# Kernel tuning notes

Measured on AMD Instinct MI355X. Metric: run time of the kernel, lower is better.

Reference implementation:

```python
import jax, jax.numpy as jnp
import numpy as np
import math

B, C, H, L, E = 4, 4, 8, 512, 128  # L == win_size + 1


def setup_inputs() -> dict:
    key = jax.random.key(0)
    kq, kk, kv, ks = jax.random.split(key, 4)
    queries = jax.random.normal(kq, (B, C, H, L, E), jnp.float32)
    keys = jax.random.normal(kk, (B, C, H, L, E), jnp.float32)
    values = jax.random.normal(kv, (B, C, H, L, E), jnp.float32)
    sigma = jax.random.normal(ks, (B, C, H, L), jnp.float32)
    # triangular causal mask: True above the diagonal (masked out)
    tri = jnp.triu(jnp.ones((L, L), dtype=bool), k=1)
    attn_mask = jnp.broadcast_to(tri[None, None, None], (B, 1, 1, L, L))
    return {"queries": queries, "keys": keys, "values": values,
            "sigma": sigma, "attn_mask": attn_mask}


def reference(queries, keys, values, sigma, attn_mask):
    Bq, Cq, Hq, Lq, Eq = queries.shape
    scale = 1.0 / math.sqrt(Eq)
    # scores: [B,C,H,L,L]
    scores = jnp.einsum("bchle,bchme->bchlm", queries, keys)
    scores = jnp.where(attn_mask, -jnp.inf, scores)
    attn = scale * scores

    # Gaussian prior from learned sigma
    sig = jax.nn.sigmoid(sigma * 5.0) + 1e-5
    sig = jnp.power(3.0, sig) - 1.0            # [B,C,H,L]
    sig = sig[..., None]                        # [B,C,H,L,1]
    idx = jnp.arange(Lq, dtype=queries.dtype)
    dist = jnp.abs(idx[:, None] - idx[None, :])  # [L,L]
    inv_norm = 1.0 / (math.sqrt(2.0 * math.pi) * sig)
    prior = inv_norm * jnp.exp(-(dist ** 2) / (2.0 * sig ** 2))  # [B,C,H,L,L]

    series = jax.nn.softmax(attn, axis=-1)      # dropout p=0.0 -> identity
    V = jnp.einsum("bchlm,bchme->bchle", series, values)
    sigma_out = jnp.broadcast_to(sig, prior.shape)
    return V, series, prior, sigma_out
```

## Files before the change

kernel.cpp:

```cpp
#include <hip/hip_runtime.h>
#include <math.h>

#define L 512
#define E 128
#define NT 8

typedef __attribute__((ext_vector_type(8))) short bf16x8;
typedef __attribute__((ext_vector_type(4))) float f32x4;
typedef __attribute__((ext_vector_type(4))) unsigned short u16x4;

__device__ __forceinline__ unsigned short bf16_rne(float x) {
  unsigned u = __builtin_bit_cast(unsigned, x);
  unsigned r = u + 0x7FFFu + ((u >> 16) & 1u);
  return (unsigned short)(r >> 16);
}
__device__ __forceinline__ float bf16_to_f(unsigned short h) {
  unsigned u = ((unsigned)h) << 16;
  return __builtin_bit_cast(float, u);
}

__global__ __launch_bounds__(256) void prior_kernel(
    const float* __restrict__ sigma,
    float* __restrict__ prior,
    float* __restrict__ sigma_out) {
  const int half = threadIdx.x >> 7;
  const int t128 = threadIdx.x & 127;
  const int m0 = t128 * 4;
#pragma unroll 4
  for (int i = 0; i < 16; ++i) {
    const int row = blockIdx.x * 32 + i * 2 + half;
    const int l = row & (L - 1);
    const float x = sigma[row];
    const float sg = 1.0f / (1.0f + __expf(-5.0f * x)) + 1e-5f;
    const float sigp = expm1f(sg * 1.0986122886681098f);
    const float inv_norm = 0.3989422804014327f / sigp;
    const float c = -1.0f / (2.0f * sigp * sigp);

    f32x4 pr, so;
    so[0] = so[1] = so[2] = so[3] = sigp;
#pragma unroll
    for (int j = 0; j < 4; ++j) {
      float d = (float)(l - (m0 + j));
      pr[j] = inv_norm * __expf(c * d * d);
    }
    const size_t off = (size_t)row * L + m0;
    __builtin_nontemporal_store(pr, (f32x4*)(prior + off));
    __builtin_nontemporal_store(so, (f32x4*)(sigma_out + off));
  }
}

__global__ __launch_bounds__(256, 2) void attn_kernel(
    const float* __restrict__ Q,
    const float* __restrict__ K,
    const float* __restrict__ V,
    float* __restrict__ outV,
    float* __restrict__ series) {
  const int bch = blockIdx.x;
  const int qt = blockIdx.y;
  const int tid = threadIdx.x;
  const int w = tid >> 6, lane = tid & 63, r = lane & 15, g = lane >> 4;

  __shared__ char smem[34816];
  char* sKhi = smem;
  char* sKlo = smem + 17408;
  char* sP = smem;
  char* sVt = smem + 9216;

  const size_t base = (size_t)bch * (L * E);
  const int qbase = qt * 64;
  const float scale = 0.08838834764831845f;

  bf16x8 qh[4], ql[4];
  {
    const float* qrow = Q + base + (size_t)(qbase + 16 * w + r) * E;
#pragma unroll
    for (int ks = 0; ks < 4; ++ks) {
      const int e0 = 32 * ks + 8 * g;
      f32x4 a = *(const f32x4*)(qrow + e0);
      f32x4 b = *(const f32x4*)(qrow + e0 + 4);
#pragma unroll
      for (int j = 0; j < 4; ++j) {
        float xa = a[j] * scale;
        unsigned short ha = bf16_rne(xa);
        qh[ks][j] = (short)ha;
        ql[ks][j] = (short)bf16_rne(xa - bf16_to_f(ha));
        float xb = b[j] * scale;
        unsigned short hb = bf16_rne(xb);
        qh[ks][4 + j] = (short)hb;
        ql[ks][4 + j] = (short)bf16_rne(xb - bf16_to_f(hb));
      }
    }
  }

  f32x4 Sacc[NT][4];
#pragma unroll
  for (int t = 0; t < NT; ++t)
#pragma unroll
    for (int cb = 0; cb < 4; ++cb) Sacc[t][cb] = (f32x4){0.f, 0.f, 0.f, 0.f};

#pragma unroll
  for (int t = 0; t < NT; ++t) {
    if (t <= qt) {
      __syncthreads();
#pragma unroll
      for (int i = 0; i < 8; ++i) {
        int f = i * 256 + tid;
        int row = f >> 5;
        int e0 = (f & 31) * 4;
        f32x4 kv = *(const f32x4*)(K + base + (size_t)(t * 64 + row) * E + e0);
        u16x4 h4, l4;
#pragma unroll
        for (int j = 0; j < 4; ++j) {
          unsigned short h = bf16_rne(kv[j]);
          h4[j] = h;
          l4[j] = bf16_rne(kv[j] - bf16_to_f(h));
        }
        *(u16x4*)(sKhi + row * 272 + e0 * 2) = h4;
        *(u16x4*)(sKlo + row * 272 + e0 * 2) = l4;
      }
      __syncthreads();

#pragma unroll
      for (int ks = 0; ks < 4; ++ks) {
#pragma unroll
        for (int cb = 0; cb < 4; ++cb) {
          const int kb = (16 * cb + r) * 272 + (32 * ks + 8 * g) * 2;
          bf16x8 bh = *(const bf16x8*)(sKhi + kb);
          bf16x8 bl = *(const bf16x8*)(sKlo + kb);
          f32x4 acc = Sacc[t][cb];
          acc = __builtin_amdgcn_mfma_f32_16x16x32_bf16(qh[ks], bh, acc, 0, 0, 0);
          acc = __builtin_amdgcn_mfma_f32_16x16x32_bf16(ql[ks], bh, acc, 0, 0, 0);
          acc = __builtin_amdgcn_mfma_f32_16x16x32_bf16(qh[ks], bl, acc, 0, 0, 0);
          Sacc[t][cb] = acc;
        }
      }
    }
  }

  float mrow[4], srow[4], inv[4];
#pragma unroll
  for (int reg = 0; reg < 4; ++reg) mrow[reg] = -__builtin_inff();

#pragma unroll
  for (int t = 0; t < NT; ++t) {
    if (t > qt) continue;
#pragma unroll
    for (int cb = 0; cb < 4; ++cb)
#pragma unroll
      for (int reg = 0; reg < 4; ++reg) {
        float s = Sacc[t][cb][reg];
        if (t == qt && (16 * cb + r) > (16 * w + 4 * g + reg))
          s = -__builtin_inff();
        Sacc[t][cb][reg] = s;
        mrow[reg] = fmaxf(mrow[reg], s);
      }
  }
#pragma unroll
  for (int off = 1; off <= 8; off <<= 1)
#pragma unroll
    for (int reg = 0; reg < 4; ++reg)
      mrow[reg] = fmaxf(mrow[reg], __shfl_xor(mrow[reg], off, 64));

#pragma unroll
  for (int reg = 0; reg < 4; ++reg) srow[reg] = 0.0f;
#pragma unroll
  for (int t = 0; t < NT; ++t) {
    if (t > qt) continue;
#pragma unroll
    for (int cb = 0; cb < 4; ++cb)
#pragma unroll
      for (int reg = 0; reg < 4; ++reg) {
        float p = __expf(Sacc[t][cb][reg] - mrow[reg]);
        Sacc[t][cb][reg] = p;
        srow[reg] += p;
      }
  }
#pragma unroll
  for (int off = 1; off <= 8; off <<= 1)
#pragma unroll
    for (int reg = 0; reg < 4; ++reg) srow[reg] += __shfl_xor(srow[reg], off, 64);
#pragma unroll
  for (int reg = 0; reg < 4; ++reg) inv[reg] = 1.0f / srow[reg];

  f32x4 Oacc[8];
#pragma unroll
  for (int cb = 0; cb < 8; ++cb) Oacc[cb] = (f32x4){0.f, 0.f, 0.f, 0.f};

#pragma unroll
  for (int t = 0; t < NT; ++t) {
    if (t <= qt) {
      __syncthreads();
#pragma unroll
      for (int cb = 0; cb < 4; ++cb)
#pragma unroll
        for (int reg = 0; reg < 4; ++reg) {
          float p = Sacc[t][cb][reg] * inv[reg];
          *(unsigned short*)(sP + (16 * w + 4 * g + reg) * 144 +
                             (16 * cb + r) * 2) = bf16_rne(p);
        }
#pragma unroll
      for (int bb = 0; bb < 2; ++bb) {
        int bidx = tid + 256 * bb;
        int m0 = (bidx >> 5) * 4;
        int e0 = (bidx & 31) * 4;
        const float* vrow = V + base + (size_t)(t * 64 + m0) * E + e0;
        f32x4 R0 = *(const f32x4*)(vrow);
        f32x4 R1 = *(const f32x4*)(vrow + E);
        f32x4 R2 = *(const f32x4*)(vrow + 2 * E);
        f32x4 R3 = *(const f32x4*)(vrow + 3 * E);
#pragma unroll
        for (int i = 0; i < 4; ++i) {
          u16x4 wv;
          wv[0] = bf16_rne(R0[i]);
          wv[1] = bf16_rne(R1[i]);
          wv[2] = bf16_rne(R2[i]);
          wv[3] = bf16_rne(R3[i]);
          int e = e0 + i;
          int byte = e * 144 + m0 * 2;
          byte ^= ((e >> 2) & 7) << 4;
          *(u16x4*)(sVt + byte) = wv;
        }
      }
      __syncthreads();

#pragma unroll
      for (int i = 0; i < 4; ++i) {
        int f = tid + 256 * i;
        int q = f >> 4, m4 = f & 15;
        u16x4 pv = *(const u16x4*)(sP + q * 144 + m4 * 8);
        f32x4 o;
        o[0] = bf16_to_f(pv[0]);
        o[1] = bf16_to_f(pv[1]);
        o[2] = bf16_to_f(pv[2]);
        o[3] = bf16_to_f(pv[3]);
        *(f32x4*)(series + ((size_t)bch * L + qbase + q) * L + t * 64 +
                  4 * m4) = o;
      }

#pragma unroll
      for (int ks = 0; ks < 2; ++ks) {
        bf16x8 ap =
            *(const bf16x8*)(sP + (16 * w + r) * 144 + (32 * ks + 8 * g) * 2);
#pragma unroll
        for (int cb = 0; cb < 8; ++cb) {
          int e = 16 * cb + r;
          int byte = e * 144 + (32 * ks + 8 * g) * 2;
          byte ^= ((e >> 2) & 7) << 4;
          bf16x8 bv = *(const bf16x8*)(sVt + byte);
          Oacc[cb] = __builtin_amdgcn_mfma_f32_16x16x32_bf16(ap, bv, Oacc[cb],
                                                             0, 0, 0);
        }
      }
    }
  }

#pragma unroll
  for (int t = 0; t < NT; ++t) {
    if (t > qt) {
      f32x4 z = (f32x4){0.f, 0.f, 0.f, 0.f};
#pragma unroll
      for (int i = 0; i < 4; ++i) {
        int f = tid + 256 * i;
        int q = f >> 4, m4 = f & 15;
        *(f32x4*)(series + ((size_t)bch * L + qbase + q) * L + t * 64 +
                  4 * m4) = z;
      }
    }
  }

#pragma unroll
  for (int cb = 0; cb < 8; ++cb)
#pragma unroll
    for (int reg = 0; reg < 4; ++reg)
      outV[base + (size_t)(qbase + 16 * w + 4 * g + reg) * E + 16 * cb + r] =
          Oacc[cb][reg];
}

extern "C" void kernel_launch(void* const* d_in, const int* in_sizes, int n_in,
                              void* d_out, int out_size, void* d_ws,
                              size_t ws_size, hipStream_t stream) {
  const float* Q = (const float*)d_in[0];
  const float* K = (const float*)d_in[1];
  const float* V = (const float*)d_in[2];
  const float* sigma = (const float*)d_in[3];

  float* out = (float*)d_out;
  float* outV = out;
  float* series = out + 8388608;
  float* prior = out + 41943040;
  float* sigma_out = out + 75497472;

  attn_kernel<<<dim3(128, NT), 256, 0, stream>>>(Q, K, V, outV, series);
  prior_kernel<<<dim3(2048), 256, 0, stream>>>(sigma, prior, sigma_out);
}
```

Before: 538.3 us.

## Pair causal query tiles per block and write fp32 series directly

```diff
diff --git a/kernel.cpp b/kernel.cpp
--- a/kernel.cpp
+++ b/kernel.cpp
@@ -56,7 +56,6 @@
     float* __restrict__ outV,
     float* __restrict__ series) {
   const int bch = blockIdx.x;
-  const int qt = blockIdx.y;
   const int tid = threadIdx.x;
   const int w = tid >> 6, lane = tid & 63, r = lane & 15, g = lane >> 4;
 
@@ -67,213 +66,212 @@
   char* sVt = smem + 9216;
 
   const size_t base = (size_t)bch * (L * E);
-  const int qbase = qt * 64;
   const float scale = 0.08838834764831845f;
 
-  bf16x8 qh[4], ql[4];
-  {
-    const float* qrow = Q + base + (size_t)(qbase + 16 * w + r) * E;
-#pragma unroll
-    for (int ks = 0; ks < 4; ++ks) {
-      const int e0 = 32 * ks + 8 * g;
-      f32x4 a = *(const f32x4*)(qrow + e0);
-      f32x4 b = *(const f32x4*)(qrow + e0 + 4);
-#pragma unroll
-      for (int j = 0; j < 4; ++j) {
-        float xa = a[j] * scale;
-        unsigned short ha = bf16_rne(xa);
-        qh[ks][j] = (short)ha;
-        ql[ks][j] = (short)bf16_rne(xa - bf16_to_f(ha));
-        float xb = b[j] * scale;
-        unsigned short hb = bf16_rne(xb);
-        qh[ks][4 + j] = (short)hb;
-        ql[ks][4 + j] = (short)bf16_rne(xb - bf16_to_f(hb));
+#pragma unroll 1
+  for (int pass = 0; pass < 2; ++pass) {
+    const int qt = pass ? 7 - blockIdx.y : blockIdx.y;
+    const int qbase = qt * 64;
+    __syncthreads();
+
+    bf16x8 qh[4], ql[4];
+    {
+      const float* qrow = Q + base + (size_t)(qbase + 16 * w + r) * E;
+#pragma unroll
+      for (int ks = 0; ks < 4; ++ks) {
+        const int e0 = 32 * ks + 8 * g;
+        f32x4 a = *(const f32x4*)(qrow + e0);
+        f32x4 b = *(const f32x4*)(qrow + e0 + 4);
+#pragma unroll
+        for (int j = 0; j < 4; ++j) {
+          float xa = a[j] * scale;
+          unsigned short ha = bf16_rne(xa);
+          qh[ks][j] = (short)ha;
+          ql[ks][j] = (short)bf16_rne(xa - bf16_to_f(ha));
+          float xb = b[j] * scale;
+          unsigned short hb = bf16_rne(xb);
+          qh[ks][4 + j] = (short)hb;
+          ql[ks][4 + j] = (short)bf16_rne(xb - bf16_to_f(hb));
+        }
       }
     }
+
+    f32x4 Sacc[NT][4];
+#pragma unroll
+    for (int t = 0; t < NT; ++t)
+#pragma unroll
+      for (int cb = 0; cb < 4; ++cb) Sacc[t][cb] = (f32x4){0.f, 0.f, 0.f, 0.f};
+
+#pragma unroll
+    for (int t = 0; t < NT; ++t) {
+      if (t <= qt) {
+        __syncthreads();
+#pragma unroll
+        for (int i = 0; i < 8; ++i) {
+          int f = i * 256 + tid;
+          int row = f >> 5;
+          int e0 = (f & 31) * 4;
+          f32x4 kv =
+              *(const f32x4*)(K + base + (size_t)(t * 64 + row) * E + e0);
+          u16x4 h4, l4;
+#pragma unroll
+          for (int j = 0; j < 4; ++j) {
+            unsigned short h = bf16_rne(kv[j]);
+            h4[j] = h;
+            l4[j] = bf16_rne(kv[j] - bf16_to_f(h));
+          }
+          *(u16x4*)(sKhi + row * 272 + e0 * 2) = h4;
+          *(u16x4*)(sKlo + row * 272 + e0 * 2) = l4;
+        }
+        __syncthreads();
+
+#pragma unroll
+        for (int ks = 0; ks < 4; ++ks) {
+#pragma unroll
+          for (int cb = 0; cb < 4; ++cb) {
+            const int kb = (16 * cb + r) * 272 + (32 * ks + 8 * g) * 2;
+            bf16x8 bh = *(const bf16x8*)(sKhi + kb);
+            bf16x8 bl = *(const bf16x8*)(sKlo + kb);
+            f32x4 acc = Sacc[t][cb];
+            acc = __builtin_amdgcn_mfma_f32_16x16x32_bf16(qh[ks], bh, acc, 0, 0, 0);
+            acc = __builtin_amdgcn_mfma_f32_16x16x32_bf16(ql[ks], bh, acc, 0, 0, 0);
+            acc = __builtin_amdgcn_mfma_f32_16x16x32_bf16(qh[ks], bl, acc, 0, 0, 0);
+            Sacc[t][cb] = acc;
+          }
+        }
+      }
+    }
+
+    float mrow[4], srow[4], inv[4];
+#pragma unroll
+    for (int reg = 0; reg < 4; ++reg) mrow[reg] = -__builtin_inff();
+
+#pragma unroll
+    for (int t = 0; t < NT; ++t) {
+      if (t > qt) continue;
+#pragma unroll
+      for (int cb = 0; cb < 4; ++cb)
+#pragma unroll
+        for (int reg = 0; reg < 4; ++reg) {
+          float s = Sacc[t][cb][reg];
+          if (t == qt && (16 * cb + r) > (16 * w + 4 * g + reg))
+            s = -__builtin_inff();
+          Sacc[t][cb][reg] = s;
+          mrow[reg] = fmaxf(mrow[reg], s);
+        }
+    }
+#pragma unroll
+    for (int off = 1; off <= 8; off <<= 1)
+#pragma unroll
+      for (int reg = 0; reg < 4; ++reg)
+        mrow[reg] = fmaxf(mrow[reg], __shfl_xor(mrow[reg], off, 64));
+
+#pragma unroll
+    for (int reg = 0; reg < 4; ++reg) srow[reg] = 0.0f;
+#pragma unroll
+    for (int t = 0; t < NT; ++t) {
+      if (t > qt) continue;
+#pragma unroll
+      for (int cb = 0; cb < 4; ++cb)
+#pragma unroll
+        for (int reg = 0; reg < 4; ++reg) {
+          float p = __expf(Sacc[t][cb][reg] - mrow[reg]);
+          Sacc[t][cb][reg] = p;
+          srow[reg] += p;
+        }
+    }
+#pragma unroll
+    for (int off = 1; off <= 8; off <<= 1)
+#pragma unroll
+      for (int reg = 0; reg < 4; ++reg)
+        srow[reg] += __shfl_xor(srow[reg], off, 64);
+#pragma unroll
+    for (int reg = 0; reg < 4; ++reg) inv[reg] = 1.0f / srow[reg];
+
+    f32x4 Oacc[8];
+#pragma unroll
+    for (int cb = 0; cb < 8; ++cb) Oacc[cb] = (f32x4){0.f, 0.f, 0.f, 0.f};
+
+#pragma unroll
+    for (int t = 0; t < NT; ++t) {
+      if (t <= qt) {
+        __syncthreads();
+#pragma unroll
+        for (int cb = 0; cb < 4; ++cb)
+#pragma unroll
+          for (int reg = 0; reg < 4; ++reg) {
+            float p = Sacc[t][cb][reg] * inv[reg];
+            *(unsigned short*)(sP + (16 * w + 4 * g + reg) * 144 +
+                               (16 * cb + r) * 2) = bf16_rne(p);
+          }
+#pragma unroll
+        for (int bb = 0; bb < 2; ++bb) {
+          int bidx = tid + 256 * bb;
+          int m0 = (bidx >> 5) * 4;
+          int e0 = (bidx & 31) * 4;
+          const float* vrow = V + base + (size_t)(t * 64 + m0) * E + e0;
+          f32x4 R0 = *(const f32x4*)(vrow);
+          f32x4 R1 = *(const f32x4*)(vrow + E);
+          f32x4 R2 = *(const f32x4*)(vrow + 2 * E);
+          f32x4 R3 = *(const f32x4*)(vrow + 3 * E);
+#pragma unroll
+          for (int i = 0; i < 4; ++i) {
+            u16x4 wv;
+            wv[0] = bf16_rne(R0[i]);
+            wv[1] = bf16_rne(R1[i]);
+            wv[2] = bf16_rne(R2[i]);
+            wv[3] = bf16_rne(R3[i]);
+            int e = e0 + i;
+            int byte = e * 144 + m0 * 2;
+            byte ^= ((e >> 2) & 7) << 4;
+            *(u16x4*)(sVt + byte) = wv;
+          }
+        }
+        __syncthreads();
+
+#pragma unroll
+        for (int cb = 0; cb < 4; ++cb)
+#pragma unroll
+          for (int reg = 0; reg < 4; ++reg) {
+            size_t off = ((size_t)bch * L + qbase + 16 * w + 4 * g + reg) * L +
+                         t * 64 + 16 * cb + r;
+            __builtin_nontemporal_store(Sacc[t][cb][reg] * inv[reg],
+                                        series + off);
+          }
+
+#pragma unroll
+        for (int ks = 0; ks < 2; ++ks) {
+          bf16x8 ap = *(const bf16x8*)(sP + (16 * w + r) * 144 +
+                                       (32 * ks + 8 * g) * 2);
+#pragma unroll
+          for (int cb = 0; cb < 8; ++cb) {
+            int e = 16 * cb + r;
+            int byte = e * 144 + (32 * ks + 8 * g) * 2;
+            byte ^= ((e >> 2) & 7) << 4;
+            bf16x8 bv = *(const bf16x8*)(sVt + byte);
+            Oacc[cb] = __builtin_amdgcn_mfma_f32_16x16x32_bf16(ap, bv, Oacc[cb],
+                                                               0, 0, 0);
+          }
+        }
+      } else {
+#pragma unroll
+        for (int cb = 0; cb < 4; ++cb)
+#pragma unroll
+          for (int reg = 0; reg < 4; ++reg) {
+            size_t off = ((size_t)bch * L + qbase + 16 * w + 4 * g + reg) * L +
+                         t * 64 + 16 * cb + r;
+            __builtin_nontemporal_store(0.0f, series + off);
+          }
+      }
+    }
+
+#pragma unroll
+    for (int cb = 0; cb < 8; ++cb)
+#pragma unroll
+      for (int reg = 0; reg < 4; ++reg)
+        outV[base + (size_t)(qbase + 16 * w + 4 * g + reg) * E + 16 * cb + r] =
+            Oacc[cb][reg];
   }
-
-  f32x4 Sacc[NT][4];
-#pragma unroll
-  for (int t = 0; t < NT; ++t)
-#pragma unroll
-    for (int cb = 0; cb < 4; ++cb) Sacc[t][cb] = (f32x4){0.f, 0.f, 0.f, 0.f};
-
-#pragma unroll
-  for (int t = 0; t < NT; ++t) {
-    if (t <= qt) {
-      __syncthreads();
-#pragma unroll
-      for (int i = 0; i < 8; ++i) {
-        int f = i * 256 + tid;
-        int row = f >> 5;
-        int e0 = (f & 31) * 4;
-        f32x4 kv = *(const f32x4*)(K + base + (size_t)(t * 64 + row) * E + e0);
-        u16x4 h4, l4;
-#pragma unroll
-        for (int j = 0; j < 4; ++j) {
-          unsigned short h = bf16_rne(kv[j]);
-          h4[j] = h;
-          l4[j] = bf16_rne(kv[j] - bf16_to_f(h));
-        }
-        *(u16x4*)(sKhi + row * 272 + e0 * 2) = h4;
-        *(u16x4*)(sKlo + row * 272 + e0 * 2) = l4;
-      }
-      __syncthreads();
-
-#pragma unroll
-      for (int ks = 0; ks < 4; ++ks) {
-#pragma unroll
-        for (int cb = 0; cb < 4; ++cb) {
-          const int kb = (16 * cb + r) * 272 + (32 * ks + 8 * g) * 2;
-          bf16x8 bh = *(const bf16x8*)(sKhi + kb);
-          bf16x8 bl = *(const bf16x8*)(sKlo + kb);
-          f32x4 acc = Sacc[t][cb];
-          acc = __builtin_amdgcn_mfma_f32_16x16x32_bf16(qh[ks], bh, acc, 0, 0, 0);
-          acc = __builtin_amdgcn_mfma_f32_16x16x32_bf16(ql[ks], bh, acc, 0, 0, 0);
-          acc = __builtin_amdgcn_mfma_f32_16x16x32_bf16(qh[ks], bl, acc, 0, 0, 0);
-          Sacc[t][cb] = acc;
-        }
-      }
-    }
-  }
-
-  float mrow[4], srow[4], inv[4];
-#pragma unroll
-  for (int reg = 0; reg < 4; ++reg) mrow[reg] = -__builtin_inff();
-
-#pragma unroll
-  for (int t = 0; t < NT; ++t) {
-    if (t > qt) continue;
-#pragma unroll
-    for (int cb = 0; cb < 4; ++cb)
-#pragma unroll
-      for (int reg = 0; reg < 4; ++reg) {
-        float s = Sacc[t][cb][reg];
-        if (t == qt && (16 * cb + r) > (16 * w + 4 * g + reg))
-          s = -__builtin_inff();
-        Sacc[t][cb][reg] = s;
-        mrow[reg] = fmaxf(mrow[reg], s);
-      }
-  }
-#pragma unroll
-  for (int off = 1; off <= 8; off <<= 1)
-#pragma unroll
-    for (int reg = 0; reg < 4; ++reg)
-      mrow[reg] = fmaxf(mrow[reg], __shfl_xor(mrow[reg], off, 64));
-
-#pragma unroll
-  for (int reg = 0; reg < 4; ++reg) srow[reg] = 0.0f;
-#pragma unroll
-  for (int t = 0; t < NT; ++t) {
-    if (t > qt) continue;
-#pragma unroll
-    for (int cb = 0; cb < 4; ++cb)
-#pragma unroll
-      for (int reg = 0; reg < 4; ++reg) {
-        float p = __expf(Sacc[t][cb][reg] - mrow[reg]);
-        Sacc[t][cb][reg] = p;
-        srow[reg] += p;
-      }
-  }
-#pragma unroll
-  for (int off = 1; off <= 8; off <<= 1)
-#pragma unroll
-    for (int reg = 0; reg < 4; ++reg) srow[reg] += __shfl_xor(srow[reg], off, 64);
-#pragma unroll
-  for (int reg = 0; reg < 4; ++reg) inv[reg] = 1.0f / srow[reg];
-
-  f32x4 Oacc[8];
-#pragma unroll
-  for (int cb = 0; cb < 8; ++cb) Oacc[cb] = (f32x4){0.f, 0.f, 0.f, 0.f};
-
-#pragma unroll
-  for (int t = 0; t < NT; ++t) {
-    if (t <= qt) {
-      __syncthreads();
-#pragma unroll
-      for (int cb = 0; cb < 4; ++cb)
-#pragma unroll
-        for (int reg = 0; reg < 4; ++reg) {
-          float p = Sacc[t][cb][reg] * inv[reg];
-          *(unsigned short*)(sP + (16 * w + 4 * g + reg) * 144 +
-                             (16 * cb + r) * 2) = bf16_rne(p);
-        }
-#pragma unroll
-      for (int bb = 0; bb < 2; ++bb) {
-        int bidx = tid + 256 * bb;
-        int m0 = (bidx >> 5) * 4;
-        int e0 = (bidx & 31) * 4;
-        const float* vrow = V + base + (size_t)(t * 64 + m0) * E + e0;
-        f32x4 R0 = *(const f32x4*)(vrow);
-        f32x4 R1 = *(const f32x4*)(vrow + E);
-        f32x4 R2 = *(const f32x4*)(vrow + 2 * E);
-        f32x4 R3 = *(const f32x4*)(vrow + 3 * E);
-#pragma unroll
-        for (int i = 0; i < 4; ++i) {
-          u16x4 wv;
-          wv[0] = bf16_rne(R0[i]);
-          wv[1] = bf16_rne(R1[i]);
-          wv[2] = bf16_rne(R2[i]);
-          wv[3] = bf16_rne(R3[i]);
-          int e = e0 + i;
-          int byte = e * 144 + m0 * 2;
-          byte ^= ((e >> 2) & 7) << 4;
-          *(u16x4*)(sVt + byte) = wv;
-        }
-      }
-      __syncthreads();
-
-#pragma unroll
-      for (int i = 0; i < 4; ++i) {
-        int f = tid + 256 * i;
-        int q = f >> 4, m4 = f & 15;
-        u16x4 pv = *(const u16x4*)(sP + q * 144 + m4 * 8);
-        f32x4 o;
-        o[0] = bf16_to_f(pv[0]);
-        o[1] = bf16_to_f(pv[1]);
-        o[2] = bf16_to_f(pv[2]);
-        o[3] = bf16_to_f(pv[3]);
-        *(f32x4*)(series + ((size_t)bch * L + qbase + q) * L + t * 64 +
-                  4 * m4) = o;
-      }
-
-#pragma unroll
-      for (int ks = 0; ks < 2; ++ks) {
-        bf16x8 ap =
-            *(const bf16x8*)(sP + (16 * w + r) * 144 + (32 * ks + 8 * g) * 2);
-#pragma unroll
-        for (int cb = 0; cb < 8; ++cb) {
-          int e = 16 * cb + r;
-          int byte = e * 144 + (32 * ks + 8 * g) * 2;
-          byte ^= ((e >> 2) & 7) << 4;
-          bf16x8 bv = *(const bf16x8*)(sVt + byte);
-          Oacc[cb] = __builtin_amdgcn_mfma_f32_16x16x32_bf16(ap, bv, Oacc[cb],
-                                                             0, 0, 0);
-        }
-      }
-    }
-  }
-
-#pragma unroll
-  for (int t = 0; t < NT; ++t) {
-    if (t > qt) {
-      f32x4 z = (f32x4){0.f, 0.f, 0.f, 0.f};
-#pragma unroll
-      for (int i = 0; i < 4; ++i) {
-        int f = tid + 256 * i;
-        int q = f >> 4, m4 = f & 15;
-        *(f32x4*)(series + ((size_t)bch * L + qbase + q) * L + t * 64 +
-                  4 * m4) = z;
-      }
-    }
-  }
-
-#pragma unroll
-  for (int cb = 0; cb < 8; ++cb)
-#pragma unroll
-    for (int reg = 0; reg < 4; ++reg)
-      outV[base + (size_t)(qbase + 16 * w + 4 * g + reg) * E + 16 * cb + r] =
-          Oacc[cb][reg];
 }
 
 extern "C" void kernel_launch(void* const* d_in, const int* in_sizes, int n_in,
@@ -290,6 +288,6 @@
   float* prior = out + 41943040;
   float* sigma_out = out + 75497472;
 
-  attn_kernel<<<dim3(128, NT), 256, 0, stream>>>(Q, K, V, outV, series);
+  attn_kernel<<<dim3(128, 4), 256, 0, stream>>>(Q, K, V, outV, series);
   prior_kernel<<<dim3(2048), 256, 0, stream>>>(sigma, prior, sigma_out);
 }
```

Result: slower. 643.7 us (+19.6%).
